# Kernel optimization log

Hardware: AMD Instinct MI355X
Metric: run time of the kernel (lower is better)

## Reference

```python
import jax, jax.numpy as jnp
import numpy as np

B, T, C = 1, 4096, 2048
NH, HS, NQG = 16, 128, 4          # n_head, head_size, n_query_groups (GQA)
Q_PER_KV = NH // NQG              # 4
QKV_DIM = (NH + 2 * NQG) * HS     # 3072
ROT = HS // 2                     # rotary half-dim = 64


def setup_inputs() -> dict:
    key = jax.random.key(0)
    k0, k1, k2 = jax.random.split(key, 3)
    x = jax.random.normal(k0, (B, T, C), dtype=jnp.float32)
    W_attn = jax.random.normal(k1, (QKV_DIM, C), dtype=jnp.float32) * 0.02
    W_proj = jax.random.normal(k2, (C, C), dtype=jnp.float32) * 0.02
    # RoPE cache: cos/sin of shape (T, head_size/2), flash-attn convention
    inv_freq = 1.0 / (10000.0 ** (jnp.arange(0, HS, 2, dtype=jnp.float32) / HS))
    freqs = jnp.arange(T, dtype=jnp.float32)[:, None] * inv_freq[None, :]
    return {"x": x, "cos": jnp.cos(freqs), "sin": jnp.sin(freqs),
            "W_attn": W_attn, "W_proj": W_proj}


def _apply_rope(t, cos, sin):
    # t: (B, T, H, HS); cos/sin: (T, ROT). Non-interleaved (rotate-half) form.
    x1, x2 = t[..., :ROT], t[..., ROT:]
    c = cos[None, :, None, :]
    s = sin[None, :, None, :]
    return jnp.concatenate([x1 * c - x2 * s, x2 * c + x1 * s], axis=-1)


def reference(x, cos, sin, W_attn, W_proj):
    Bx, Tx, Cx = x.shape
    qkv = jnp.einsum('btc,fc->btf', x, W_attn)                 # (B,T,3072)
    qkv = qkv.reshape(Bx, Tx, NQG, Q_PER_KV + 2, HS)
    q = qkv[:, :, :, :Q_PER_KV, :].reshape(Bx, Tx, NH, HS)     # (B,T,16,128)
    k = qkv[:, :, :, Q_PER_KV, :]                              # (B,T,4,128)
    v = qkv[:, :, :, Q_PER_KV + 1, :]                          # (B,T,4,128)
    q = _apply_rope(q, cos, sin)
    k = _apply_rope(k, cos, sin)
    # GQA: expand kv groups to match query heads (repeat_interleave on head dim)
    k = jnp.repeat(k, Q_PER_KV, axis=2)                        # (B,T,16,128)
    v = jnp.repeat(v, Q_PER_KV, axis=2)
    scale = 1.0 / np.sqrt(HS).astype(np.float32)
    scores = jnp.einsum('bthd,bshd->bhts', q, k) * scale       # (B,H,T,T)
    causal = jnp.tril(jnp.ones((Tx, Tx), dtype=bool))
    scores = jnp.where(causal[None, None], scores, jnp.finfo(scores.dtype).min)
    attn = jax.nn.softmax(scores, axis=-1)
    y = jnp.einsum('bhts,bshd->bthd', attn, v).reshape(Bx, Tx, Cx)
    return jnp.einsum('btc,oc->bto', y, W_proj)
```

## Files before the change

### kernel.cpp

```cpp
#include <hip/hip_runtime.h>
#include <hip/hip_bf16.h>

typedef __hip_bfloat16 bf16;
typedef __attribute__((ext_vector_type(8))) short short8;
typedef __attribute__((ext_vector_type(4))) short short4v;
typedef __attribute__((ext_vector_type(4))) float floatx4;

#define T_SEQ 4096
#define C_DIM 2048
#define NHEAD 16
#define HSZ   128
#define NGRP  4

#define MFMA_BF16(A,B,C) __builtin_amdgcn_mfma_f32_16x16x32_bf16((A),(B),(C),0,0,0)

__device__ __forceinline__ void gld_lds16(const bf16* g, bf16* l) {
  __builtin_amdgcn_global_load_lds(
      (__attribute__((address_space(1))) void*)(g),
      (__attribute__((address_space(3))) void*)(l), 16, 0, 0);
}

__global__ void cvt_kernel(const float* __restrict__ src, bf16* __restrict__ dst, long n)
{
  const long i = ((long)blockIdx.x * blockDim.x + threadIdx.x) * 8;
  if (i >= n) return;
  const float4 a = *(const float4*)(src + i);
  const float4 b = *(const float4*)(src + i + 4);
  bf16 tmp[8];
  tmp[0] = __float2bfloat16(a.x); tmp[1] = __float2bfloat16(a.y);
  tmp[2] = __float2bfloat16(a.z); tmp[3] = __float2bfloat16(a.w);
  tmp[4] = __float2bfloat16(b.x); tmp[5] = __float2bfloat16(b.y);
  tmp[6] = __float2bfloat16(b.z); tmp[7] = __float2bfloat16(b.w);
  *(short8*)(dst + i) = *(const short8*)tmp;
}

__global__ __launch_bounds__(256, 2)
void gemm_bt_kernel(const bf16* __restrict__ A, const bf16* __restrict__ B,
                    float* __restrict__ Cf, bf16* __restrict__ Cq,
                    bf16* __restrict__ Ck, bf16* __restrict__ Cvt,
                    int K, int qkv_mode)
{
  __shared__ alignas(16) bf16 As[128 * 64];
  __shared__ alignas(16) bf16 Bs[128 * 64];

  const int t  = threadIdx.x;
  const int w  = t >> 6, l = t & 63;
  const int wr = w >> 1, wc = w & 1;
  const int q4 = l >> 4, ln = l & 15;
  const long bm = (long)blockIdx.y * 128;
  const long bn = (long)blockIdx.x * 128;

  floatx4 acc[4][4] = {};

  const bf16* Ab = A + (bm + t / 8) * (long)K + (t % 8) * 8;
  const bf16* Bb = B + (bn + t / 8) * (long)K + (t % 8) * 8;

  for (int k0 = 0; k0 < K; k0 += 64) {
    __syncthreads();
#pragma unroll
    for (int i = 0; i < 4; ++i) {
      gld_lds16(Ab + (long)i * 32 * K + k0, As + (i * 256 + w * 64) * 8);
      gld_lds16(Bb + (long)i * 32 * K + k0, Bs + (i * 256 + w * 64) * 8);
    }
    __syncthreads();
#pragma unroll
    for (int kk = 0; kk < 64; kk += 32) {
      short8 af[4], bfr[4];
      const int co = kk + q4 * 8;
#pragma unroll
      for (int mi = 0; mi < 4; ++mi)
        af[mi] = *(const short8*)(As + (wr * 64 + mi * 16 + ln) * 64 + co);
#pragma unroll
      for (int ni = 0; ni < 4; ++ni)
        bfr[ni] = *(const short8*)(Bs + (wc * 64 + ni * 16 + ln) * 64 + co);
#pragma unroll
      for (int mi = 0; mi < 4; ++mi)
#pragma unroll
        for (int ni = 0; ni < 4; ++ni)
          acc[mi][ni] = MFMA_BF16(af[mi], bfr[ni], acc[mi][ni]);
    }
  }

  if (!qkv_mode) {
#pragma unroll
    for (int mi = 0; mi < 4; ++mi) {
      const long r0 = bm + wr * 64 + mi * 16 + q4 * 4;
#pragma unroll
      for (int ni = 0; ni < 4; ++ni) {
        const long c = bn + wc * 64 + ni * 16 + ln;
#pragma unroll
        for (int r = 0; r < 4; ++r)
          Cf[(r0 + r) * C_DIM + c] = acc[mi][ni][r];
      }
    }
  } else {
    const int cb = blockIdx.x;
    const int g = cb / 6, slot = cb - g * 6;
    if (slot == 5) {
      bf16* dstv = Cvt + (long)g * HSZ * T_SEQ;
#pragma unroll
      for (int mi = 0; mi < 4; ++mi) {
        const long r0 = bm + wr * 64 + mi * 16 + q4 * 4;
#pragma unroll
        for (int ni = 0; ni < 4; ++ni) {
          const long c = wc * 64 + ni * 16 + ln;
          short4v pk;
#pragma unroll
          for (int r = 0; r < 4; ++r) {
            bf16 v = __float2bfloat16(acc[mi][ni][r]);
            pk[r] = *(short*)&v;
          }
          *(short4v*)(dstv + c * T_SEQ + r0) = pk;
        }
      }
    } else {
      bf16* dst = (slot < 4) ? (Cq + (long)(g * 4 + slot) * T_SEQ * HSZ)
                             : (Ck + (long)g * T_SEQ * HSZ);
#pragma unroll
      for (int mi = 0; mi < 4; ++mi) {
        const long r0 = bm + wr * 64 + mi * 16 + q4 * 4;
#pragma unroll
        for (int ni = 0; ni < 4; ++ni) {
          const long c = wc * 64 + ni * 16 + ln;
#pragma unroll
          for (int r = 0; r < 4; ++r)
            dst[(r0 + r) * HSZ + c] = __float2bfloat16(acc[mi][ni][r]);
        }
      }
    }
  }
}

__global__ void rope_kernel(bf16* __restrict__ Q, bf16* __restrict__ Kb,
                            const float* __restrict__ cs, const float* __restrict__ sn)
{
  const long idx = (long)blockIdx.x * blockDim.x + threadIdx.x;
  const long NQ = (long)NHEAD * T_SEQ * 64;
  bf16* buf; long rem; float qs;
  if (idx < NQ) { buf = Q;  rem = idx;      qs = 0.08838834764831845f * 1.4426950408889634f; }
  else          { buf = Kb; rem = idx - NQ; qs = 1.0f; }
  const int d  = (int)(rem & 63);
  const int tt = (int)((rem >> 6) & (T_SEQ - 1));
  const int hh = (int)(rem >> 18);
  const float c = cs[tt * 64 + d];
  const float s = sn[tt * 64 + d];
  bf16* p = buf + ((long)hh * T_SEQ + tt) * HSZ + d;
  const float x1 = __bfloat162float(p[0]);
  const float x2 = __bfloat162float(p[64]);
  p[0]  = __float2bfloat16((x1 * c - x2 * s) * qs);
  p[64] = __float2bfloat16((x2 * c + x1 * s) * qs);
}

__global__ __launch_bounds__(256, 2)
void attn_kernel(const bf16* __restrict__ Qg, const bf16* __restrict__ Kg,
                 const bf16* __restrict__ Vtg, bf16* __restrict__ Y)
{
  __shared__ alignas(16) bf16 Ks[64][132];
  __shared__ alignas(16) bf16 Vt[128][68];
  __shared__ alignas(16) bf16 Ps[128][68];

  const int h = blockIdx.y;
  const int p = (blockIdx.y < 8) ? blockIdx.x : (31 - blockIdx.x);
  const int g = h >> 2;
  const int t = threadIdx.x;
  const int w = t >> 6, l = t & 63;
  const int q4 = l >> 4, ln = l & 15;

  const bf16* Qh = Qg + (long)h * T_SEQ * HSZ;
  const bf16* Kh = Kg + (long)g * T_SEQ * HSZ;
  const bf16* Vh = Vtg + (long)g * HSZ * T_SEQ;

  const int qbase = p * 128 + w * 32;

  short8 qf[2][4];
#pragma unroll
  for (int mi = 0; mi < 2; ++mi) {
    const long row = qbase + mi * 16 + ln;
#pragma unroll
    for (int ks = 0; ks < 4; ++ks)
      qf[mi][ks] = *(const short8*)(Qh + row * HSZ + ks * 32 + q4 * 8);
  }

  short8 ones_f;
#pragma unroll
  for (int i = 0; i < 8; ++i) ones_f[i] = (ln == 0) ? (short)0x3F80 : (short)0;

  floatx4 acc[2][8] = {};
  floatx4 acc_l[2] = {};

  const int krow = t >> 4, kc = (t & 15) * 8;
  const int vrow = t >> 3, vc = (t & 7) * 8;

  short8 kpre[4], vpre[4];
#pragma unroll
  for (int i = 0; i < 4; ++i) {
    kpre[i] = *(const short8*)(Kh + (long)(krow + 16 * i) * HSZ + kc);
    vpre[i] = *(const short8*)(Vh + (long)(vrow + 32 * i) * T_SEQ + vc);
  }

  const int jmax = 2 * p + 1;
  for (int j = 0; j <= jmax; ++j) {
    const int s0 = j * 64;
#pragma unroll
    for (int i = 0; i < 4; ++i) {
      *(short8*)(&Ks[krow + 16 * i][kc]) = kpre[i];
      *(short8*)(&Vt[vrow + 32 * i][vc]) = vpre[i];
    }
    __syncthreads();
    if (j < jmax) {
      const int s1 = s0 + 64;
#pragma unroll
      for (int i = 0; i < 4; ++i) {
        kpre[i] = *(const short8*)(Kh + (long)(s1 + krow + 16 * i) * HSZ + kc);
        vpre[i] = *(const short8*)(Vh + (long)(vrow + 32 * i) * T_SEQ + s1 + vc);
      }
    }

    floatx4 sacc[2][4] = {};
#pragma unroll
    for (int ks = 0; ks < 4; ++ks) {
      short8 kf[4];
#pragma unroll
      for (int ni = 0; ni < 4; ++ni)
        kf[ni] = *(const short8*)(&Ks[ni * 16 + ln][ks * 32 + q4 * 8]);
#pragma unroll
      for (int mi = 0; mi < 2; ++mi)
#pragma unroll
        for (int ni = 0; ni < 4; ++ni)
          sacc[mi][ni] = MFMA_BF16(qf[mi][ks], kf[ni], sacc[mi][ni]);
    }

#pragma unroll
    for (int mi = 0; mi < 2; ++mi) {
      const int base_m = qbase + mi * 16 + q4 * 4 - s0 - ln;
#pragma unroll
      for (int ni = 0; ni < 4; ++ni)
#pragma unroll
        for (int r = 0; r < 4; ++r) {
          float pv = __builtin_amdgcn_exp2f(sacc[mi][ni][r]);
          if (base_m + r - ni * 16 < 0) pv = 0.f;
          Ps[w * 32 + mi * 16 + q4 * 4 + r][ni * 16 + ln] = __float2bfloat16(pv);
        }
    }

#pragma unroll
    for (int ks = 0; ks < 2; ++ks) {
      short8 pf[2], vf[8];
#pragma unroll
      for (int mi = 0; mi < 2; ++mi)
        pf[mi] = *(const short8*)(&Ps[w * 32 + mi * 16 + ln][ks * 32 + q4 * 8]);
#pragma unroll
      for (int nd = 0; nd < 8; ++nd)
        vf[nd] = *(const short8*)(&Vt[nd * 16 + ln][ks * 32 + q4 * 8]);
#pragma unroll
      for (int mi = 0; mi < 2; ++mi) {
        acc_l[mi] = MFMA_BF16(pf[mi], ones_f, acc_l[mi]);
#pragma unroll
        for (int nd = 0; nd < 8; ++nd)
          acc[mi][nd] = MFMA_BF16(pf[mi], vf[nd], acc[mi][nd]);
      }
    }
    __syncthreads();
  }

#pragma unroll
  for (int mi = 0; mi < 2; ++mi) {
#pragma unroll
    for (int r = 0; r < 4; ++r) {
      const float lv = __shfl(acc_l[mi][r], l & 48, 64);
      const float inv = (lv > 0.f) ? 1.f / lv : 0.f;
      const long tq = qbase + mi * 16 + q4 * 4 + r;
#pragma unroll
      for (int nd = 0; nd < 8; ++nd)
        Y[tq * C_DIM + h * HSZ + nd * 16 + ln] = __float2bfloat16(acc[mi][nd][r] * inv);
    }
  }
}

extern "C" void kernel_launch(void* const* d_in, const int* in_sizes, int n_in,
                              void* d_out, int out_size, void* d_ws, size_t ws_size,
                              hipStream_t stream)
{
  const float* x  = (const float*)d_in[0];
  const float* cs = (const float*)d_in[1];
  const float* sn = (const float*)d_in[2];
  const float* Wa = (const float*)d_in[3];
  const float* Wp = (const float*)d_in[4];
  float* out = (float*)d_out;

  const long nx  = (long)T_SEQ * C_DIM;
  const long nwa = (long)(NHEAD + 2 * NGRP) * HSZ * C_DIM;
  const long nwp = (long)C_DIM * C_DIM;
  const long nqh = (long)NHEAD * T_SEQ * HSZ;
  const long nkg = (long)NGRP * T_SEQ * HSZ;

  const size_t need = (size_t)(nx + nwa + nqh + 2 * nkg + nqh) * sizeof(bf16);
  if (ws_size < need) return;

  bf16* xb  = (bf16*)d_ws;
  bf16* Wab = xb + nx;
  bf16* Q   = Wab + nwa;
  bf16* K   = Q + nqh;
  bf16* Vt  = K + nkg;
  bf16* Y   = Vt + nkg;
  bf16* Wpb = xb;

  cvt_kernel<<<(int)(nx  / 8 / 256), 256, 0, stream>>>(x,  xb,  nx);
  cvt_kernel<<<(int)(nwa / 8 / 256), 256, 0, stream>>>(Wa, Wab, nwa);
  gemm_bt_kernel<<<dim3(24, 32), 256, 0, stream>>>(xb, Wab, nullptr, Q, K, Vt, C_DIM, 1);
  rope_kernel<<<20480, 256, 0, stream>>>(Q, K, cs, sn);
  attn_kernel<<<dim3(32, NHEAD), 256, 0, stream>>>(Q, K, Vt, Y);
  cvt_kernel<<<(int)(nwp / 8 / 256), 256, 0, stream>>>(Wp, Wpb, nwp);
  gemm_bt_kernel<<<dim3(16, 32), 256, 0, stream>>>(Y, Wpb, out, nullptr, nullptr, nullptr, C_DIM, 0);
}
```

Baseline: 349.7 us.

## Stage V-transpose stores via LDS, vectorize RoPE, skip masked attention tiles

The V-transpose epilogue of the QKV GEMM now goes through shared memory in two passes, so global writes become coalesced 16-byte rows instead of strided 8-byte stores. The RoPE kernel processes 8 elements per thread with vector loads of cos/sin and Q/K, using an eighth as many blocks. In attention, each wave skips the QK, softmax and PV work for key tiles that lie entirely above its causal diagonal. The GEMM launch bounds are raised to 3 blocks per SM, which may force more register pressure or spills.

```diff
diff --git a/kernel.cpp b/kernel.cpp
--- a/kernel.cpp
+++ b/kernel.cpp
@@ -34,7 +34,7 @@
   *(short8*)(dst + i) = *(const short8*)tmp;
 }
 
-__global__ __launch_bounds__(256, 2)
+__global__ __launch_bounds__(256, 3)
 void gemm_bt_kernel(const bf16* __restrict__ A, const bf16* __restrict__ B,
                     float* __restrict__ Cf, bf16* __restrict__ Cq,
                     bf16* __restrict__ Ck, bf16* __restrict__ Cvt,
@@ -99,19 +99,31 @@
     if (slot == 5) {
       bf16* dstv = Cvt + (long)g * HSZ * T_SEQ;
 #pragma unroll
-      for (int mi = 0; mi < 4; ++mi) {
-        const long r0 = bm + wr * 64 + mi * 16 + q4 * 4;
-#pragma unroll
-        for (int ni = 0; ni < 4; ++ni) {
-          const long c = wc * 64 + ni * 16 + ln;
-          short4v pk;
-#pragma unroll
-          for (int r = 0; r < 4; ++r) {
-            bf16 v = __float2bfloat16(acc[mi][ni][r]);
-            pk[r] = *(short*)&v;
+      for (int pass = 0; pass < 2; ++pass) {
+        __syncthreads();
+        if (wc == pass) {
+#pragma unroll
+          for (int mi = 0; mi < 4; ++mi) {
+            const int tc = wr * 64 + mi * 16 + q4 * 4;
+#pragma unroll
+            for (int ni = 0; ni < 4; ++ni) {
+              const int dr = ni * 16 + ln;
+              short4v pk;
+#pragma unroll
+              for (int r = 0; r < 4; ++r) {
+                bf16 v = __float2bfloat16(acc[mi][ni][r]);
+                pk[r] = *(short*)&v;
+              }
+              *(short4v*)(As + dr * 128 + tc) = pk;
+            }
           }
-          *(short4v*)(dstv + c * T_SEQ + r0) = pk;
         }
+        __syncthreads();
+        const int row = t >> 2, ch = (t & 3) * 32;
+        bf16* gp = dstv + (long)(pass * 64 + row) * T_SEQ + bm + ch;
+#pragma unroll
+        for (int jj = 0; jj < 4; ++jj)
+          *(short8*)(gp + jj * 8) = *(const short8*)(As + row * 128 + ch + jj * 8);
       }
     } else {
       bf16* dst = (slot < 4) ? (Cq + (long)(g * 4 + slot) * T_SEQ * HSZ)
@@ -135,20 +147,34 @@
                             const float* __restrict__ cs, const float* __restrict__ sn)
 {
   const long idx = (long)blockIdx.x * blockDim.x + threadIdx.x;
-  const long NQ = (long)NHEAD * T_SEQ * 64;
+  const long NQ = (long)NHEAD * T_SEQ * 8;
   bf16* buf; long rem; float qs;
   if (idx < NQ) { buf = Q;  rem = idx;      qs = 0.08838834764831845f * 1.4426950408889634f; }
   else          { buf = Kb; rem = idx - NQ; qs = 1.0f; }
-  const int d  = (int)(rem & 63);
-  const int tt = (int)((rem >> 6) & (T_SEQ - 1));
-  const int hh = (int)(rem >> 18);
-  const float c = cs[tt * 64 + d];
-  const float s = sn[tt * 64 + d];
-  bf16* p = buf + ((long)hh * T_SEQ + tt) * HSZ + d;
-  const float x1 = __bfloat162float(p[0]);
-  const float x2 = __bfloat162float(p[64]);
-  p[0]  = __float2bfloat16((x1 * c - x2 * s) * qs);
-  p[64] = __float2bfloat16((x2 * c + x1 * s) * qs);
+  const int d0 = (int)(rem & 7) * 8;
+  const int tt = (int)((rem >> 3) & (T_SEQ - 1));
+  const int hh = (int)(rem >> 15);
+  const float4 c0 = *(const float4*)(cs + tt * 64 + d0);
+  const float4 c1 = *(const float4*)(cs + tt * 64 + d0 + 4);
+  const float4 s0 = *(const float4*)(sn + tt * 64 + d0);
+  const float4 s1 = *(const float4*)(sn + tt * 64 + d0 + 4);
+  float cc[8] = {c0.x,c0.y,c0.z,c0.w,c1.x,c1.y,c1.z,c1.w};
+  float ss[8] = {s0.x,s0.y,s0.z,s0.w,s1.x,s1.y,s1.z,s1.w};
+  bf16* p = buf + ((long)hh * T_SEQ + tt) * HSZ + d0;
+  short8 v1 = *(const short8*)(p);
+  short8 v2 = *(const short8*)(p + 64);
+  short8 o1, o2;
+#pragma unroll
+  for (int jj = 0; jj < 8; ++jj) {
+    short u1 = v1[jj], u2 = v2[jj];
+    const float x1 = __bfloat162float(*(bf16*)&u1);
+    const float x2 = __bfloat162float(*(bf16*)&u2);
+    bf16 y1 = __float2bfloat16((x1 * cc[jj] - x2 * ss[jj]) * qs);
+    bf16 y2 = __float2bfloat16((x2 * cc[jj] + x1 * ss[jj]) * qs);
+    o1[jj] = *(short*)&y1; o2[jj] = *(short*)&y2;
+  }
+  *(short8*)(p)      = o1;
+  *(short8*)(p + 64) = o2;
 }
 
 __global__ __launch_bounds__(256, 2)
@@ -216,48 +242,50 @@
       }
     }
 
-    floatx4 sacc[2][4] = {};
-#pragma unroll
-    for (int ks = 0; ks < 4; ++ks) {
-      short8 kf[4];
-#pragma unroll
-      for (int ni = 0; ni < 4; ++ni)
-        kf[ni] = *(const short8*)(&Ks[ni * 16 + ln][ks * 32 + q4 * 8]);
-#pragma unroll
-      for (int mi = 0; mi < 2; ++mi)
+    if (s0 <= qbase + 31) {
+      floatx4 sacc[2][4] = {};
+#pragma unroll
+      for (int ks = 0; ks < 4; ++ks) {
+        short8 kf[4];
 #pragma unroll
         for (int ni = 0; ni < 4; ++ni)
-          sacc[mi][ni] = MFMA_BF16(qf[mi][ks], kf[ni], sacc[mi][ni]);
-    }
-
-#pragma unroll
-    for (int mi = 0; mi < 2; ++mi) {
-      const int base_m = qbase + mi * 16 + q4 * 4 - s0 - ln;
-#pragma unroll
-      for (int ni = 0; ni < 4; ++ni)
-#pragma unroll
-        for (int r = 0; r < 4; ++r) {
-          float pv = __builtin_amdgcn_exp2f(sacc[mi][ni][r]);
-          if (base_m + r - ni * 16 < 0) pv = 0.f;
-          Ps[w * 32 + mi * 16 + q4 * 4 + r][ni * 16 + ln] = __float2bfloat16(pv);
+          kf[ni] = *(const short8*)(&Ks[ni * 16 + ln][ks * 32 + q4 * 8]);
+#pragma unroll
+        for (int mi = 0; mi < 2; ++mi)
+#pragma unroll
+          for (int ni = 0; ni < 4; ++ni)
+            sacc[mi][ni] = MFMA_BF16(qf[mi][ks], kf[ni], sacc[mi][ni]);
+      }
+
+#pragma unroll
+      for (int mi = 0; mi < 2; ++mi) {
+        const int base_m = qbase + mi * 16 + q4 * 4 - s0 - ln;
+#pragma unroll
+        for (int ni = 0; ni < 4; ++ni)
+#pragma unroll
+          for (int r = 0; r < 4; ++r) {
+            float pv = __builtin_amdgcn_exp2f(sacc[mi][ni][r]);
+            if (base_m + r - ni * 16 < 0) pv = 0.f;
+            Ps[w * 32 + mi * 16 + q4 * 4 + r][ni * 16 + ln] = __float2bfloat16(pv);
+          }
+      }
+
+#pragma unroll
+      for (int ks = 0; ks < 2; ++ks) {
+        short8 pf[2], vf[8];
+#pragma unroll
+        for (int mi = 0; mi < 2; ++mi)
+          pf[mi] = *(const short8*)(&Ps[w * 32 + mi * 16 + ln][ks * 32 + q4 * 8]);
+#pragma unroll
+        for (int nd = 0; nd < 8; ++nd)
+          vf[nd] = *(const short8*)(&Vt[nd * 16 + ln][ks * 32 + q4 * 8]);
+#pragma unroll
+        for (int mi = 0; mi < 2; ++mi) {
+          acc_l[mi] = MFMA_BF16(pf[mi], ones_f, acc_l[mi]);
+#pragma unroll
+          for (int nd = 0; nd < 8; ++nd)
+            acc[mi][nd] = MFMA_BF16(pf[mi], vf[nd], acc[mi][nd]);
         }
-    }
-
-#pragma unroll
-    for (int ks = 0; ks < 2; ++ks) {
-      short8 pf[2], vf[8];
-#pragma unroll
-      for (int mi = 0; mi < 2; ++mi)
-        pf[mi] = *(const short8*)(&Ps[w * 32 + mi * 16 + ln][ks * 32 + q4 * 8]);
-#pragma unroll
-      for (int nd = 0; nd < 8; ++nd)
-        vf[nd] = *(const short8*)(&Vt[nd * 16 + ln][ks * 32 + q4 * 8]);
-#pragma unroll
-      for (int mi = 0; mi < 2; ++mi) {
-        acc_l[mi] = MFMA_BF16(pf[mi], ones_f, acc_l[mi]);
-#pragma unroll
-        for (int nd = 0; nd < 8; ++nd)
-          acc[mi][nd] = MFMA_BF16(pf[mi], vf[nd], acc[mi][nd]);
       }
     }
     __syncthreads();
@@ -308,7 +336,7 @@
   cvt_kernel<<<(int)(nx  / 8 / 256), 256, 0, stream>>>(x,  xb,  nx);
   cvt_kernel<<<(int)(nwa / 8 / 256), 256, 0, stream>>>(Wa, Wab, nwa);
   gemm_bt_kernel<<<dim3(24, 32), 256, 0, stream>>>(xb, Wab, nullptr, Q, K, Vt, C_DIM, 1);
-  rope_kernel<<<20480, 256, 0, stream>>>(Q, K, cs, sn);
+  rope_kernel<<<2560, 256, 0, stream>>>(Q, K, cs, sn);
   attn_kernel<<<dim3(32, NHEAD), 256, 0, stream>>>(Q, K, Vt, Y);
   cvt_kernel<<<(int)(nwp / 8 / 256), 256, 0, stream>>>(Wp, Wpb, nwp);
   gemm_bt_kernel<<<dim3(16, 32), 256, 0, stream>>>(Y, Wpb, out, nullptr, nullptr, nullptr, C_DIM, 0);
```

Result: no change. 347.0 us (-0.8%).
